# Kernel optimization log

Measured on AMD Instinct MI355X. Metric: run time of the kernel, lower is better.

## Reference

```python
import jax, jax.numpy as jnp
import numpy as np

N_ATOMS = 100_000
N_PAIRS = 6_400_000
N_BATCH = 16


def smooth_switch(x, x0, x1):
    t = (x - x0) / (x1 - x0)
    tc = jnp.clip(t, 1e-9, 1.0 - 1e-9)  # safe interior values
    f1 = jnp.exp(-1.0 / tc)
    f2 = jnp.exp(-1.0 / (1.0 - tc))
    s = f1 / (f1 + f2)
    return jnp.where(t <= 0.0, 0.0, jnp.where(t >= 1.0, 1.0, s))


def setup_inputs() -> dict:
    key = jax.random.key(0)
    k1, k2, k3, k4, k5 = jax.random.split(key, 5)
    atomic_numbers = jax.random.randint(k1, (N_ATOMS,), 1, 81).astype(jnp.float32)
    # displacements scaled so distances span the (0, 10) switch window
    displacements = jax.random.normal(k2, (N_PAIRS, 3), dtype=jnp.float32) * 2.5
    idx_i = jnp.sort(jax.random.randint(k3, (N_PAIRS,), 0, N_ATOMS)).astype(jnp.int32)
    idx_j = jax.random.randint(k4, (N_PAIRS,), 0, N_ATOMS).astype(jnp.int32)
    atom_mask = jnp.ones((N_ATOMS,), dtype=jnp.float32)
    batch_mask = jnp.ones((N_PAIRS,), dtype=jnp.float32)
    batch_segments = jnp.sort(jax.random.randint(k5, (N_ATOMS,), 0, N_BATCH)).astype(jnp.int32)
    # ZBL parameters (non-trainable constants in the module)
    a_coefficient = jnp.asarray(0.8854, dtype=jnp.float32)
    a_exponent = jnp.asarray(0.23, dtype=jnp.float32)
    phi_coefficients = jnp.asarray([0.18175, 0.50986, 0.28022, 0.02817], dtype=jnp.float32)
    phi_exponents = jnp.asarray([3.1998, 0.94229, 0.4029, 0.20162], dtype=jnp.float32)
    return {
        "atomic_numbers": atomic_numbers,
        "displacements": displacements,
        "idx_i": idx_i,
        "idx_j": idx_j,
        "atom_mask": atom_mask,
        "batch_mask": batch_mask,
        "batch_segments": batch_segments,
        "batch_size": N_BATCH,
        "a_coefficient": a_coefficient,
        "a_exponent": a_exponent,
        "phi_coefficients": phi_coefficients,
        "phi_exponents": phi_exponents,
    }


def reference(atomic_numbers, displacements, idx_i, idx_j, atom_mask, batch_mask,
              batch_segments, batch_size, a_coefficient, a_exponent,
              phi_coefficients, phi_exponents):
    n_atoms = atomic_numbers.shape[0]
    displacements = displacements + (1.0 - batch_mask[..., None])
    distances = jnp.maximum(jnp.linalg.norm(displacements, axis=-1), 1e-10)  # [P]
    switch_off = smooth_switch(distances, 0.0, 10.0)

    safe_atomic_numbers = jnp.maximum(atomic_numbers, 1e-06)
    za = jnp.exp(jnp.log(safe_atomic_numbers) * jnp.abs(a_exponent))
    za = jnp.nan_to_num(za, nan=1e-06, posinf=1e6, neginf=1e-06)
    za_sum = za[idx_i] + za[idx_j]                     # [P]
    denominator = jnp.maximum(za_sum, 1e-06)
    a_ij = jnp.abs(a_coefficient) / denominator
    a_ij = jnp.nan_to_num(a_ij, nan=1e-06, posinf=1e6, neginf=1e-06)
    arguments = jnp.maximum(distances, 1e-10) / jnp.maximum(a_ij, 1e-10)
    arguments = jnp.nan_to_num(arguments, nan=1e-06, posinf=1e6, neginf=1e-06)

    raw_coefficients = jnp.abs(phi_coefficients)
    coefficients = raw_coefficients / jnp.maximum(jnp.sum(raw_coefficients), 1e-10)
    exponents = jnp.maximum(jnp.abs(phi_exponents), 1e-10)
    log_terms = -exponents[None, :] * arguments[:, None]          # [P,4]
    max_log = jnp.max(log_terms, axis=1, keepdims=True)           # [P,1]
    exp_terms = jnp.exp(log_terms - max_log)
    exp_terms = jnp.nan_to_num(exp_terms, nan=0.0, posinf=1.0, neginf=0.0)
    phi = jnp.sum(coefficients[None, :] * exp_terms, axis=1) * jnp.exp(max_log)[..., 0]
    phi = jnp.maximum(phi, 1e-30)
    phi = jnp.nan_to_num(phi, nan=1e-30, posinf=1e6, neginf=1e-30)

    safe_distances = jnp.maximum(distances, 1e-10)
    safe_phi = jnp.maximum(phi, 1e-30)
    safe_switch = jnp.maximum(switch_off, 1e-30)
    charge_product = jnp.minimum(safe_atomic_numbers[idx_i] * safe_atomic_numbers[idx_j], 1e4)
    base_repulsion = jnp.minimum(0.5 * charge_product / safe_distances, 1e6)
    repulsion = base_repulsion * safe_phi * safe_switch
    repulsion = jnp.clip(repulsion, 0.0, 1e6)
    repulsion = jnp.nan_to_num(repulsion, nan=0.0, posinf=1e6, neginf=0.0)
    repulsion = repulsion * batch_mask

    Erep = jax.ops.segment_sum(repulsion, segment_ids=idx_i, num_segments=n_atoms)
    Erep = Erep * atom_mask
    Erep = jnp.clip(Erep, 0.0, 1e6)
    Erep = jnp.nan_to_num(Erep, nan=0.0, posinf=1e6, neginf=0.0)
    Erep = Erep * 0.01
    return Erep[..., None, None, None]  # [N,1,1,1]
```

## Files before the change

kernel.cpp:

```cpp
#include <hip/hip_runtime.h>
#include <math.h>


#define LOG2E 1.4426950408889634f
#define BLK   1024
#define NBLK  256
#define STRD  (2 * BLK)

static __device__ __forceinline__ float rcpf_(float x)  { return __builtin_amdgcn_rcpf(x); }
static __device__ __forceinline__ float rsqf_(float x)  { return __builtin_amdgcn_rsqf(x); }
static __device__ __forceinline__ float exp2f_(float x) { return __builtin_amdgcn_exp2f(x); }
static __device__ __forceinline__ float log2f_(float x) { return __builtin_amdgcn_logf(x); }

struct f3 { float x, y, z; };
struct G  { int ii, jj; float bm, dx, dy, dz; };

__global__ void zbl_k0(const float* __restrict__ an,
                       unsigned char* __restrict__ z8,
                       float* __restrict__ out, int n) {
    int i = blockIdx.x * blockDim.x + threadIdx.x;
    if (i >= n) return;
    int z = (int)(an[i] + 0.5f);
    z8[i] = (unsigned char)min(max(z, 1), 255);
    out[i] = 0.0f;
}

static __device__ __forceinline__ G loadG(const int* __restrict__ idx_i,
                                          const int* __restrict__ idx_j,
                                          const float* __restrict__ bmk,
                                          const float* __restrict__ disp,
                                          int p, int cend) {
    G g; g.ii = -1; g.jj = 0; g.bm = 0.0f; g.dx = 0.0f; g.dy = 0.0f; g.dz = 0.0f;
    if (p < cend) {
        g.ii = idx_i[p];
        g.jj = idx_j[p];
        g.bm = bmk[p];
        f3 d = *reinterpret_cast<const f3*>(disp + (long)p * 3);
        g.dx = d.x; g.dy = d.y; g.dz = d.z;
    }
    return g;
}

__global__ __launch_bounds__(BLK) void zbl_pair_kernel(
    const float* __restrict__ disp,
    const int*   __restrict__ idx_i,
    const int*   __restrict__ idx_j,
    const float* __restrict__ batch_mask,
    const unsigned char* __restrict__ z8g,
    const float* __restrict__ a_coef_ptr,
    const float* __restrict__ a_exp_ptr,
    const float* __restrict__ phi_c,
    const float* __restrict__ phi_e,
    float* __restrict__ out_acc,
    int nA, int nP)
{
    extern __shared__ unsigned char smem[];
    const int nA_pad = (nA + 15) & ~15;
    unsigned char* s_z8 = smem;
    float*         s_za = (float*)(smem + nA_pad);

    const int tid = threadIdx.x;

    {
        const int nw = nA >> 4;
        const uint4* g4 = reinterpret_cast<const uint4*>(z8g);
        uint4* s4 = reinterpret_cast<uint4*>(s_z8);
        for (int i = tid; i < nw; i += BLK) s4[i] = g4[i];
        for (int i = (nw << 4) + tid; i < nA; i += BLK) s_z8[i] = z8g[i];
    }
    if (tid < 256) {
        float ae = fabsf(a_exp_ptr[0]);
        int z = max(tid, 1);
        s_za[tid] = exp2f_(ae * log2f_((float)z));
    }
    __syncthreads();

    const float ac_inv = rcpf_(fmaxf(fabsf(a_coef_ptr[0]), 1e-10f));
    float c0 = fabsf(phi_c[0]), c1 = fabsf(phi_c[1]);
    float c2 = fabsf(phi_c[2]), c3 = fabsf(phi_c[3]);
    const float cinv = rcpf_(fmaxf(c0 + c1 + c2 + c3, 1e-10f));
    c0 *= cinv; c1 *= cinv; c2 *= cinv; c3 *= cinv;
    const float e0 = fmaxf(fabsf(phi_e[0]), 1e-10f);
    const float e1 = fmaxf(fabsf(phi_e[1]), 1e-10f);
    const float e2 = fmaxf(fabsf(phi_e[2]), 1e-10f);
    const float e3 = fmaxf(fabsf(phi_e[3]), 1e-10f);

    const int chunk = (nP + NBLK - 1) / NBLK;
    const int cbeg  = blockIdx.x * chunk;
    const int cend  = min(cbeg + chunk, nP);
    const int lane  = tid & 63;

#define COMPUTE_G(g, rep, key)                                                  \
    {                                                                           \
        rep = 0.0f; key = -1;                                                   \
        if ((g).ii >= 0) {                                                      \
            const int zi = (int)s_z8[(g).ii];                                   \
            const int zj = (int)s_z8[(g).jj];                                   \
            const float za_i = s_za[zi];                                        \
            const float za_j = s_za[zj];                                        \
            const float add = 1.0f - (g).bm;                                    \
            const float dx = (g).dx + add, dy = (g).dy + add, dz = (g).dz + add;\
            float d2   = fmaxf(dx * dx + dy * dy + dz * dz, 1e-20f);            \
            float rsq  = rsqf_(d2);                                             \
            float dist = d2 * rsq;                                              \
            float tt = dist * 0.1f;                                             \
            float tc = fminf(fmaxf(tt, 1e-9f), 1.0f - 1e-9f);                   \
            float u  = (1.0f - 2.0f * tc) * rcpf_(tc - tc * tc);                \
            float s  = rcpf_(1.0f + exp2f_(u * LOG2E));                         \
            float sw = (tt >= 1.0f) ? 1.0f : s;                                 \
            float za_sum = za_i + za_j;                                         \
            float arg  = fminf(dist * za_sum * ac_inv, 1e6f);                   \
            float narg = -arg * LOG2E;                                          \
            float phi  = c0 * exp2f_(e0 * narg) + c1 * exp2f_(e1 * narg) +      \
                         c2 * exp2f_(e2 * narg) + c3 * exp2f_(e3 * narg);       \
            phi = fminf(fmaxf(phi, 1e-30f), 1e6f);                              \
            float cp   = fminf((float)(zi * zj), 1e4f);                         \
            float brep = fminf(0.5f * cp * rsq, 1e6f);                          \
            float r    = brep * phi * fmaxf(sw, 1e-30f);                        \
            r = fminf(fmaxf(r, 0.0f), 1e6f);                                    \
            if (!(r == r)) r = 0.0f;                                            \
            rep = r * (g).bm;                                                   \
            key = (g).ii;                                                       \
        }                                                                       \
    }

#define REDUCE_G(rep, key)                                                      \
    {                                                                           \
        const int k0_ = __shfl(key, 0);                                         \
        if (__all(key == k0_)) {                                                \
            float v = rep;                                                      \
            _Pragma("unroll")                                                   \
            for (int d = 1; d < 64; d <<= 1) v += __shfl_xor(v, d);             \
            if (lane == 0 && k0_ >= 0) atomicAdd(&out_acc[k0_], v);             \
        } else {                                                                \
            float v = rep;                                                      \
            int   k = key;                                                      \
            _Pragma("unroll")                                                   \
            for (int d = 1; d < 64; d <<= 1) {                                  \
                float nv = __shfl_down(v, d);                                   \
                int   nk = __shfl_down(k, d);                                   \
                if (lane + d < 64 && nk == k) v += nv;                          \
            }                                                                   \
            int pk = __shfl_up(k, 1);                                           \
            bool head = (lane == 0) || (pk != k);                               \
            if (head && k >= 0) atomicAdd(&out_acc[k], v);                      \
        }                                                                       \
    }

    G a0 = loadG(idx_i, idx_j, batch_mask, disp, cbeg + tid,            cend);
    G b0 = loadG(idx_i, idx_j, batch_mask, disp, cbeg + BLK + tid,      cend);
    G a1 = loadG(idx_i, idx_j, batch_mask, disp, cbeg + STRD + tid,     cend);
    G b1 = loadG(idx_i, idx_j, batch_mask, disp, cbeg + STRD + BLK + tid, cend);

    for (int pb = cbeg; pb < cend; pb += STRD) {
        G a2 = loadG(idx_i, idx_j, batch_mask, disp, pb + 2 * STRD + tid,       cend);
        G b2 = loadG(idx_i, idx_j, batch_mask, disp, pb + 2 * STRD + BLK + tid, cend);

        float repA, repB; int keyA, keyB;
        COMPUTE_G(a0, repA, keyA);
        COMPUTE_G(b0, repB, keyB);
        REDUCE_G(repA, keyA);
        REDUCE_G(repB, keyB);

        a0 = a1; b0 = b1; a1 = a2; b1 = b2;
    }
#undef COMPUTE_G
#undef REDUCE_G
}

__global__ void zbl_epilogue(float* __restrict__ out,
                             const float* __restrict__ atom_mask, int n) {
    int i = blockIdx.x * blockDim.x + threadIdx.x;
    if (i >= n) return;
    float v = out[i] * atom_mask[i];
    v = fminf(fmaxf(v, 0.0f), 1e6f);
    if (!(v == v)) v = 0.0f;
    out[i] = v * 0.01f;
}

extern "C" void kernel_launch(void* const* d_in, const int* in_sizes, int n_in,
                              void* d_out, int out_size, void* d_ws, size_t ws_size,
                              hipStream_t stream) {
    const float* an         = (const float*)d_in[0];
    const float* disp       = (const float*)d_in[1];
    const int*   idx_i      = (const int*)d_in[2];
    const int*   idx_j      = (const int*)d_in[3];
    const float* atom_mask  = (const float*)d_in[4];
    const float* batch_mask = (const float*)d_in[5];
    const float* a_coef     = (const float*)d_in[8];
    const float* a_exp      = (const float*)d_in[9];
    const float* phi_c      = (const float*)d_in[10];
    const float* phi_e      = (const float*)d_in[11];

    const int nA = in_sizes[0];
    const int nP = in_sizes[2];
    float* out = (float*)d_out;

    unsigned char* z8 = (unsigned char*)d_ws;

    zbl_k0<<<(nA + 255) / 256, 256, 0, stream>>>(an, z8, out, nA);

    const int nA_pad = (nA + 15) & ~15;
    const size_t smem = (size_t)nA_pad + 256 * sizeof(float);
    zbl_pair_kernel<<<NBLK, BLK, smem, stream>>>(
        disp, idx_i, idx_j, batch_mask, z8, a_coef, a_exp, phi_c, phi_e,
        out, nA, nP);

    zbl_epilogue<<<(nA + 255) / 256, 256, 0, stream>>>(out, atom_mask, nA);
}
```

Measured before the change: 45.12 us.

## Drop per-block LDS staging of atomic numbers; gather from global with prefetch

Measured after the change: 56.83 us. 1.26x slower.

```diff
diff --git a/kernel.cpp b/kernel.cpp
--- a/kernel.cpp
+++ b/kernel.cpp
@@ -3,8 +3,8 @@
 
 
 #define LOG2E 1.4426950408889634f
-#define BLK   1024
-#define NBLK  256
+#define BLK   256
+#define NBLK  2048
 #define STRD  (2 * BLK)
 
 static __device__ __forceinline__ float rcpf_(float x)  { return __builtin_amdgcn_rcpf(x); }
@@ -41,7 +41,7 @@
     return g;
 }
 
-__global__ __launch_bounds__(BLK) void zbl_pair_kernel(
+__global__ __launch_bounds__(BLK, 6) void zbl_pair_kernel(
     const float* __restrict__ disp,
     const int*   __restrict__ idx_i,
     const int*   __restrict__ idx_j,
@@ -52,23 +52,12 @@
     const float* __restrict__ phi_c,
     const float* __restrict__ phi_e,
     float* __restrict__ out_acc,
-    int nA, int nP)
+    int nP)
 {
-    extern __shared__ unsigned char smem[];
-    const int nA_pad = (nA + 15) & ~15;
-    unsigned char* s_z8 = smem;
-    float*         s_za = (float*)(smem + nA_pad);
-
+    __shared__ float s_za[256];
     const int tid = threadIdx.x;
 
     {
-        const int nw = nA >> 4;
-        const uint4* g4 = reinterpret_cast<const uint4*>(z8g);
-        uint4* s4 = reinterpret_cast<uint4*>(s_z8);
-        for (int i = tid; i < nw; i += BLK) s4[i] = g4[i];
-        for (int i = (nw << 4) + tid; i < nA; i += BLK) s_z8[i] = z8g[i];
-    }
-    if (tid < 256) {
         float ae = fabsf(a_exp_ptr[0]);
         int z = max(tid, 1);
         s_za[tid] = exp2f_(ae * log2f_((float)z));
@@ -85,17 +74,16 @@
     const float e2 = fmaxf(fabsf(phi_e[2]), 1e-10f);
     const float e3 = fmaxf(fabsf(phi_e[3]), 1e-10f);
 
-    const int chunk = (nP + NBLK - 1) / NBLK;
-    const int cbeg  = blockIdx.x * chunk;
-    const int cend  = min(cbeg + chunk, nP);
-    const int lane  = tid & 63;
-
-#define COMPUTE_G(g, rep, key)                                                  \
+    int chunk = (nP + NBLK - 1) / NBLK;
+    chunk = (chunk + STRD - 1) & ~(STRD - 1);
+    const int cbeg = blockIdx.x * chunk;
+    const int cend = min(cbeg + chunk, nP);
+    const int lane = tid & 63;
+
+#define COMPUTE_G(g, zi, zj, rep, key)                                          \
     {                                                                           \
         rep = 0.0f; key = -1;                                                   \
         if ((g).ii >= 0) {                                                      \
-            const int zi = (int)s_z8[(g).ii];                                   \
-            const int zj = (int)s_z8[(g).jj];                                   \
             const float za_i = s_za[zi];                                        \
             const float za_j = s_za[zj];                                        \
             const float add = 1.0f - (g).bm;                                    \
@@ -114,7 +102,7 @@
             float phi  = c0 * exp2f_(e0 * narg) + c1 * exp2f_(e1 * narg) +      \
                          c2 * exp2f_(e2 * narg) + c3 * exp2f_(e3 * narg);       \
             phi = fminf(fmaxf(phi, 1e-30f), 1e6f);                              \
-            float cp   = fminf((float)(zi * zj), 1e4f);                         \
+            float cp   = fminf((float)((zi) * (zj)), 1e4f);                     \
             float brep = fminf(0.5f * cp * rsq, 1e6f);                          \
             float r    = brep * phi * fmaxf(sw, 1e-30f);                        \
             r = fminf(fmaxf(r, 0.0f), 1e6f);                                    \
@@ -147,22 +135,30 @@
         }                                                                       \
     }
 
-    G a0 = loadG(idx_i, idx_j, batch_mask, disp, cbeg + tid,            cend);
-    G b0 = loadG(idx_i, idx_j, batch_mask, disp, cbeg + BLK + tid,      cend);
-    G a1 = loadG(idx_i, idx_j, batch_mask, disp, cbeg + STRD + tid,     cend);
+    G a0 = loadG(idx_i, idx_j, batch_mask, disp, cbeg + tid,              cend);
+    G b0 = loadG(idx_i, idx_j, batch_mask, disp, cbeg + BLK + tid,        cend);
+    G a1 = loadG(idx_i, idx_j, batch_mask, disp, cbeg + STRD + tid,       cend);
     G b1 = loadG(idx_i, idx_j, batch_mask, disp, cbeg + STRD + BLK + tid, cend);
+    int zia0 = 1, zja0 = 1, zib0 = 1, zjb0 = 1;
+    if (a0.ii >= 0) { zia0 = (int)z8g[a0.ii]; zja0 = (int)z8g[a0.jj]; }
+    if (b0.ii >= 0) { zib0 = (int)z8g[b0.ii]; zjb0 = (int)z8g[b0.jj]; }
 
     for (int pb = cbeg; pb < cend; pb += STRD) {
         G a2 = loadG(idx_i, idx_j, batch_mask, disp, pb + 2 * STRD + tid,       cend);
         G b2 = loadG(idx_i, idx_j, batch_mask, disp, pb + 2 * STRD + BLK + tid, cend);
 
+        int zia1 = 1, zja1 = 1, zib1 = 1, zjb1 = 1;
+        if (a1.ii >= 0) { zia1 = (int)z8g[a1.ii]; zja1 = (int)z8g[a1.jj]; }
+        if (b1.ii >= 0) { zib1 = (int)z8g[b1.ii]; zjb1 = (int)z8g[b1.jj]; }
+
         float repA, repB; int keyA, keyB;
-        COMPUTE_G(a0, repA, keyA);
-        COMPUTE_G(b0, repB, keyB);
+        COMPUTE_G(a0, zia0, zja0, repA, keyA);
+        COMPUTE_G(b0, zib0, zjb0, repB, keyB);
         REDUCE_G(repA, keyA);
         REDUCE_G(repB, keyB);
 
         a0 = a1; b0 = b1; a1 = a2; b1 = b2;
+        zia0 = zia1; zja0 = zja1; zib0 = zib1; zjb0 = zjb1;
     }
 #undef COMPUTE_G
 #undef REDUCE_G
@@ -199,12 +195,8 @@
     unsigned char* z8 = (unsigned char*)d_ws;
 
     zbl_k0<<<(nA + 255) / 256, 256, 0, stream>>>(an, z8, out, nA);
-
-    const int nA_pad = (nA + 15) & ~15;
-    const size_t smem = (size_t)nA_pad + 256 * sizeof(float);
-    zbl_pair_kernel<<<NBLK, BLK, smem, stream>>>(
+    zbl_pair_kernel<<<NBLK, BLK, 0, stream>>>(
         disp, idx_i, idx_j, batch_mask, z8, a_coef, a_exp, phi_c, phi_e,
-        out, nA, nP);
-
+        out, nP);
     zbl_epilogue<<<(nA + 255) / 256, 256, 0, stream>>>(out, atom_mask, nA);
 }
```
